# Performance work log

Measured on AMD Instinct MI355X. Metric: run time of the kernel, lower is better.

## Reference

```python
import jax, jax.numpy as jnp
import numpy as np

B = 131072
IN_DIM = 100
H = 256


def setup_inputs() -> dict:
    key = jax.random.key(0)
    ks = jax.random.split(key, 7)
    return {
        "x": jax.random.normal(ks[0], (B, IN_DIM), dtype=jnp.float32),
        "C": jax.random.normal(ks[1], (B, H), dtype=jnp.float32),
        "h": jax.random.normal(ks[2], (B, H), dtype=jnp.float32),
        # stacked gate weights, gate order: i, f, g, o  (equivalent to 8 separate Linears)
        "Wx": jax.random.normal(ks[3], (IN_DIM, 4 * H), dtype=jnp.float32) * 0.05,
        "Wh": jax.random.normal(ks[4], (H, 4 * H), dtype=jnp.float32) * 0.05,
        "bx": jax.random.normal(ks[5], (4 * H,), dtype=jnp.float32) * 0.05,
        "bh": jax.random.normal(ks[6], (4 * H,), dtype=jnp.float32) * 0.05,
    }


def reference(x, C, h, Wx, Wh, bx, bh):
    # two fused GEMMs replace the 8 per-gate Linears (same math)
    gates = (x @ Wx + bx) + (h @ Wh + bh)  # [B, 4H]
    i_pre, f_pre, g_pre, o_pre = jnp.split(gates, 4, axis=-1)
    i = jax.nn.sigmoid(i_pre)
    f = jax.nn.sigmoid(f_pre)
    g = jnp.tanh(g_pre)
    o = jax.nn.sigmoid(o_pre)
    c_out = f * C + i * g
    h_out = o * jnp.tanh(c_out)
    return (c_out, h_out)
```

## Files before the change

### kernel.cpp

```cpp
#include <hip/hip_runtime.h>
#include <stdint.h>


typedef short bf16x8 __attribute__((ext_vector_type(8)));
typedef float f32x4  __attribute__((ext_vector_type(4)));

#define HDIM   256
#define INDIM  100
#define NROWS  131072
#define BT_OFF 0
#define XB_OFF (1048576 / 2)
#define HB_OFF (35651584 / 2)
#define ABUF(b) ((b) * 8192)
#define BBUF(b) (24576 + (b) * 16384)

__device__ __forceinline__ float fexp(float x) {
  return __builtin_amdgcn_exp2f(x * 1.44269504088896340736f);
}
__device__ __forceinline__ float frcp(float x) { return __builtin_amdgcn_rcpf(x); }
__device__ __forceinline__ float sigm(float x) { return frcp(1.0f + fexp(-x)); }
__device__ __forceinline__ float tanh_fast(float x) {
  return 1.0f - 2.0f * frcp(1.0f + fexp(2.0f * x));
}
__device__ __forceinline__ unsigned short f2bf_rne(float f) {
  union { float f; uint32_t u; } v; v.f = f;
  return (unsigned short)((v.u + 0x7FFFu + ((v.u >> 16) & 1u)) >> 16);
}
__device__ __forceinline__ void gl16(const void* g, void* l) {
  __builtin_amdgcn_global_load_lds(
      (const __attribute__((address_space(1))) unsigned int*)g,
      (__attribute__((address_space(3))) unsigned int*)l, 16, 0, 0);
}
#define VMW(N) asm volatile("s_waitcnt vmcnt(" #N ")" ::: "memory")

__global__ void prep_all(const float* __restrict__ X, const float* __restrict__ Hin,
                         const float* __restrict__ Wx, const float* __restrict__ Wh,
                         const float* __restrict__ bxp, const float* __restrict__ bhp,
                         unsigned short* __restrict__ ws) {
  const int b = blockIdx.x, tid = threadIdx.x;
  if (b < 8192) {
    const int t   = b * 256 + tid;
    const int row = t >> 4, k0 = (t & 15) * 8;
    const float* xp = X + (size_t)row * INDIM;
    float4 lo = make_float4(0.f, 0.f, 0.f, 0.f);
    float4 hi = make_float4(0.f, 0.f, 0.f, 0.f);
    if (k0 + 4 <= INDIM) lo = *reinterpret_cast<const float4*>(xp + k0);
    if (k0 + 8 <= INDIM) hi = *reinterpret_cast<const float4*>(xp + k0 + 4);
    float va[8] = {lo.x, lo.y, lo.z, lo.w, hi.x, hi.y, hi.z, hi.w};
    unsigned short o[8];
#pragma unroll
    for (int e = 0; e < 8; ++e) {
      const int k = k0 + e;
      const float f = (k < INDIM) ? va[e] : (k == 127 ? 1.0f : 0.0f);
      o[e] = f2bf_rne(f);
    }
    *reinterpret_cast<bf16x8*>(ws + XB_OFF + (size_t)row * 128 + k0) =
        *reinterpret_cast<bf16x8*>(o);
  } else if (b < 24576) {
    const int t   = (b - 8192) * 256 + tid;
    const int row = t >> 5, k0 = (t & 31) * 8;
    const float* hp = Hin + (size_t)row * HDIM + k0;
    const float4 lo = *reinterpret_cast<const float4*>(hp);
    const float4 hi = *reinterpret_cast<const float4*>(hp + 4);
    unsigned short o[8] = {f2bf_rne(lo.x), f2bf_rne(lo.y), f2bf_rne(lo.z),
                           f2bf_rne(lo.w), f2bf_rne(hi.x), f2bf_rne(hi.y),
                           f2bf_rne(hi.z), f2bf_rne(hi.w)};
    *reinterpret_cast<bf16x8*>(ws + HB_OFF + (size_t)row * 256 + k0) =
        *reinterpret_cast<bf16x8*>(o);
  } else {
    const int unit = (b - 24576) * 4 + (tid >> 6);
    const int lane = tid & 63;
    const int kst  = unit % 12;
    const int fidb = unit / 12;
    const int bn   = fidb >> 3, fid = fidb & 7;
    const int g    = fid >> 1,  wc  = fid & 1;
    const int wcol = g * HDIM + bn * 32 + wc * 16 + (lane & 15);
    const int kb   = kst * 32 + (lane >> 4) * 8;
    unsigned short v[8];
#pragma unroll
    for (int e = 0; e < 8; ++e) {
      const int k = kb + e;
      float f = 0.0f;
      if (k < INDIM)     f = Wx[(size_t)k * 1024 + wcol];
      else if (k == 127) f = bxp[wcol] + bhp[wcol];
      else if (k >= 128) f = Wh[(size_t)(k - 128) * 1024 + wcol];
      v[e] = f2bf_rne(f);
    }
    *reinterpret_cast<bf16x8*>(ws + BT_OFF + (size_t)unit * 512 + lane * 8) =
        *reinterpret_cast<bf16x8*>(v);
  }
}

__global__ __launch_bounds__(512, 2)
void lstm_main(const unsigned short* __restrict__ ws,
               const float* __restrict__ Cin, float* __restrict__ out)
{
  __shared__ unsigned char smem[73728];

  const int tid  = threadIdx.x;
  const int orig = blockIdx.x;
  const int lg   = ((orig & 7) << 9) | (orig >> 3);
  const int mt   = lg >> 2;
  const int bnn  = lg & 3;

  const int lane = tid & 63;
  const int l15  = lane & 15;
  const int kq   = lane >> 4;
  const int wid  = tid >> 6;
  const int wr   = wid >> 2;
  const int wcq  = wid & 3;
  const int ch   = bnn * 64 + wcq * 16 + l15;
  const int sx   = (l15 >> 1) & 3;

  const unsigned short* xb = ws + XB_OFF;
  const unsigned short* hb = ws + HB_OFF;
  const unsigned short* Bt = ws + BT_OFF;

  const int ci = wid * 64 + lane;
  const int r  = ci >> 2;
  const int sc = (ci & 3) ^ ((r >> 1) & 3);
  const unsigned short* xsrc = xb + (size_t)(mt * 128 + r) * 128 + sc * 8;
  const unsigned short* hsrc = hb + (size_t)(mt * 128 + r) * 256 + sc * 8;

  const unsigned short* bsrc[2];
#pragma unroll
  for (int j = 0; j < 2; ++j) {
    const int u  = wid * 2 + j;
    const int gu = (bnn * 2 + (u >> 3)) * 8 + (u & 7);
    bsrc[j] = Bt + (size_t)gu * 12 * 512 + lane * 8;
  }
  const int adst = wid * 1024;
  const int bd0  = (wid * 2 + 0) * 1024;
  const int bd1  = (wid * 2 + 1) * 1024;

  f32x4 acc[4][4];
#pragma unroll
  for (int m = 0; m < 4; ++m)
#pragma unroll
    for (int g = 0; g < 4; ++g)
#pragma unroll
      for (int e = 0; e < 4; ++e) acc[m][g][e] = 0.0f;

  float cvv[4][4];

  auto STAGE = [&](int T) {
    char* Ad = (char*)smem + ABUF(T % 3);
    char* Bd = (char*)smem + BBUF(T % 3);
    if (T < 4) gl16(xsrc + T * 32, Ad + adst);
    else       gl16(hsrc + (T - 4) * 32, Ad + adst);
    gl16(bsrc[0] + T * 512, Bd + bd0);
    gl16(bsrc[1] + T * 512, Bd + bd1);
  };

  auto COMPUTE = [&](int S) {
    const unsigned short* Ab = (const unsigned short*)(smem + ABUF(S % 3));
    const unsigned short* Bb = (const unsigned short*)(smem + BBUF(S % 3));
    bf16x8 afr[4], bfr[4];
#pragma unroll
    for (int m = 0; m < 4; ++m)
      afr[m] = *reinterpret_cast<const bf16x8*>(
          Ab + (wr * 64 + m * 16 + l15) * 32 + ((kq ^ sx) * 8));
#pragma unroll
    for (int g = 0; g < 4; ++g) {
      const int ub = (wcq >> 1) * 8 + g * 2 + (wcq & 1);
      bfr[g] = *reinterpret_cast<const bf16x8*>(Bb + ub * 512 + lane * 8);
    }
#pragma unroll
    for (int m = 0; m < 4; ++m)
#pragma unroll
      for (int g = 0; g < 4; ++g)
        acc[m][g] = __builtin_amdgcn_mfma_f32_16x16x32_bf16(
            afr[m], bfr[g], acc[m][g], 0, 0, 0);
  };

  STAGE(0);
  STAGE(1);

#define STEP(S, KN)                                               \
  do {                                                            \
    VMW(KN);                                                      \
    __builtin_amdgcn_s_barrier();                                 \
    if ((S) + 2 < 12) STAGE((S) + 2);                             \
    if ((S) == 7) {                                               \
      const float* cb =                                           \
          Cin + ((size_t)mt * 128 + wr * 64 + kq * 4) * HDIM + ch;\
      _Pragma("unroll")                                           \
      for (int m = 0; m < 4; ++m)                                 \
        _Pragma("unroll")                                         \
        for (int e = 0; e < 4; ++e)                               \
          cvv[m][e] = __builtin_nontemporal_load(                 \
              cb + (size_t)(m * 16 + e) * HDIM);                  \
    }                                                             \
    COMPUTE(S);                                                   \
  } while (0)

  STEP(0, 3);  STEP(1, 3);  STEP(2, 3);  STEP(3, 3);
  STEP(4, 3);  STEP(5, 3);  STEP(6, 3);  STEP(7, 3);
  STEP(8, 19); STEP(9, 19); STEP(10, 3); STEP(11, 0);
#undef STEP

  float* op  = out + ((size_t)mt * 128 + wr * 64 + kq * 4) * HDIM + ch;
  float* op2 = op + (size_t)NROWS * HDIM;
#pragma unroll
  for (int m = 0; m < 4; ++m) {
#pragma unroll
    for (int e = 0; e < 4; ++e) {
      const float pi = acc[m][0][e];
      const float pf = acc[m][1][e];
      const float pg = acc[m][2][e];
      const float po = acc[m][3][e];
      const float ig = sigm(pi), fg = sigm(pf);
      const float gg = tanh_fast(pg), og = sigm(po);
      const float co = fg * cvv[m][e] + ig * gg;
      const float ho = og * tanh_fast(co);
      __builtin_nontemporal_store(co, op  + (size_t)(m * 16 + e) * HDIM);
      __builtin_nontemporal_store(ho, op2 + (size_t)(m * 16 + e) * HDIM);
    }
  }
}

extern "C" void kernel_launch(void* const* d_in, const int* in_sizes, int n_in,
                              void* d_out, int out_size, void* d_ws, size_t ws_size,
                              hipStream_t stream) {
  const float* x  = (const float*)d_in[0];
  const float* C  = (const float*)d_in[1];
  const float* h  = (const float*)d_in[2];
  const float* Wx = (const float*)d_in[3];
  const float* Wh = (const float*)d_in[4];
  const float* bx = (const float*)d_in[5];
  const float* bh = (const float*)d_in[6];
  float* o = (float*)d_out;
  unsigned short* ws = (unsigned short*)d_ws;

  prep_all<<<dim3(24768), dim3(256), 0, stream>>>(x, h, Wx, Wh, bx, bh, ws);
  lstm_main<<<dim3(4096), dim3(512), 0, stream>>>(ws, C, o);
}
```

Baseline: 193.5 us.

## Switch main GEMM to 32x32x16 MFMA with 4-wave blocks

Replaces the 16x16x32 bf16 MFMA tiles with 32x32x16 tiles, so each wave now computes a 64x32 output per gate. Blocks shrink from 8 to 4 waves, and the weight prepack layout is changed to match the new B-fragment order. Each wave issues more global-to-LDS loads per stage, and the wait counts and C prefetch step are adjusted to fit. The aim is fewer LDS fragment reads per FLOP and better MFMA throughput, at the cost of more accumulator registers per wave and fewer waves per block.

```diff
diff --git a/kernel.cpp b/kernel.cpp
--- a/kernel.cpp
+++ b/kernel.cpp
@@ -3,7 +3,7 @@
 
 
 typedef short bf16x8 __attribute__((ext_vector_type(8)));
-typedef float f32x4  __attribute__((ext_vector_type(4)));
+typedef float f32x16 __attribute__((ext_vector_type(16)));
 
 #define HDIM   256
 #define INDIM  100
@@ -70,12 +70,11 @@
   } else {
     const int unit = (b - 24576) * 4 + (tid >> 6);
     const int lane = tid & 63;
-    const int kst  = unit % 12;
-    const int fidb = unit / 12;
-    const int bn   = fidb >> 3, fid = fidb & 7;
-    const int g    = fid >> 1,  wc  = fid & 1;
-    const int wcol = g * HDIM + bn * 32 + wc * 16 + (lane & 15);
-    const int kb   = kst * 32 + (lane >> 4) * 8;
+    const int kst  = unit % 24;
+    const int g    = (unit / 24) & 3;
+    const int hb32 = unit / 96;
+    const int wcol = g * HDIM + hb32 * 32 + (lane & 31);
+    const int kb   = kst * 16 + (lane >> 5) * 8;
     unsigned short v[8];
 #pragma unroll
     for (int e = 0; e < 8; ++e) {
@@ -91,7 +90,7 @@
   }
 }
 
-__global__ __launch_bounds__(512, 2)
+__global__ __launch_bounds__(256, 2)
 void lstm_main(const unsigned short* __restrict__ ws,
                const float* __restrict__ Cin, float* __restrict__ out)
 {
@@ -104,117 +103,136 @@
   const int bnn  = lg & 3;
 
   const int lane = tid & 63;
-  const int l15  = lane & 15;
-  const int kq   = lane >> 4;
+  const int l31  = lane & 31;
+  const int kh   = lane >> 5;
   const int wid  = tid >> 6;
-  const int wr   = wid >> 2;
-  const int wcq  = wid & 3;
-  const int ch   = bnn * 64 + wcq * 16 + l15;
-  const int sx   = (l15 >> 1) & 3;
+  const int wr   = wid >> 1;
+  const int wc   = wid & 1;
+  const int ch   = bnn * 64 + wc * 32 + l31;
+  const int sx   = (l31 >> 1) & 3;
 
   const unsigned short* xb = ws + XB_OFF;
   const unsigned short* hb = ws + HB_OFF;
   const unsigned short* Bt = ws + BT_OFF;
 
-  const int ci = wid * 64 + lane;
-  const int r  = ci >> 2;
-  const int sc = (ci & 3) ^ ((r >> 1) & 3);
-  const unsigned short* xsrc = xb + (size_t)(mt * 128 + r) * 128 + sc * 8;
-  const unsigned short* hsrc = hb + (size_t)(mt * 128 + r) * 256 + sc * 8;
-
-  const unsigned short* bsrc[2];
+  const unsigned short* xsrc[2];
+  const unsigned short* hsrc[2];
 #pragma unroll
   for (int j = 0; j < 2; ++j) {
-    const int u  = wid * 2 + j;
-    const int gu = (bnn * 2 + (u >> 3)) * 8 + (u & 7);
-    bsrc[j] = Bt + (size_t)gu * 12 * 512 + lane * 8;
-  }
-  const int adst = wid * 1024;
-  const int bd0  = (wid * 2 + 0) * 1024;
-  const int bd1  = (wid * 2 + 1) * 1024;
-
-  f32x4 acc[4][4];
-#pragma unroll
-  for (int m = 0; m < 4; ++m)
+    const int ci = (wid * 2 + j) * 64 + lane;
+    const int r  = ci >> 2;
+    const int sc = (ci & 3) ^ ((r >> 1) & 3);
+    xsrc[j] = xb + (size_t)(mt * 128 + r) * 128 + sc * 8;
+    hsrc[j] = hb + (size_t)(mt * 128 + r) * 256 + sc * 8;
+  }
+  const int ad0 = (wid * 2 + 0) * 1024;
+  const int ad1 = (wid * 2 + 1) * 1024;
+
+  const unsigned short* bsrc[4];
+#pragma unroll
+  for (int j = 0; j < 4; ++j) {
+    const int lu = wid * 4 + j;
+    const int nb = lu >> 3, g = (lu >> 1) & 3, kk = lu & 1;
+    bsrc[j] = Bt + ((size_t)(((bnn * 2 + nb) * 4 + g) * 24) + kk) * 512 +
+              lane * 8;
+  }
+
+  f32x16 acc[2][4];
+#pragma unroll
+  for (int m = 0; m < 2; ++m)
 #pragma unroll
     for (int g = 0; g < 4; ++g)
 #pragma unroll
-      for (int e = 0; e < 4; ++e) acc[m][g][e] = 0.0f;
-
-  float cvv[4][4];
+      for (int e = 0; e < 16; ++e) acc[m][g][e] = 0.0f;
+
+  float cvv[2][16];
 
   auto STAGE = [&](int T) {
     char* Ad = (char*)smem + ABUF(T % 3);
     char* Bd = (char*)smem + BBUF(T % 3);
-    if (T < 4) gl16(xsrc + T * 32, Ad + adst);
-    else       gl16(hsrc + (T - 4) * 32, Ad + adst);
-    gl16(bsrc[0] + T * 512, Bd + bd0);
-    gl16(bsrc[1] + T * 512, Bd + bd1);
+    if (T < 4) {
+      gl16(xsrc[0] + T * 32, Ad + ad0);
+      gl16(xsrc[1] + T * 32, Ad + ad1);
+    } else {
+      gl16(hsrc[0] + (T - 4) * 32, Ad + ad0);
+      gl16(hsrc[1] + (T - 4) * 32, Ad + ad1);
+    }
+#pragma unroll
+    for (int j = 0; j < 4; ++j)
+      gl16(bsrc[j] + T * 1024, Bd + (wid * 4 + j) * 1024);
   };
 
   auto COMPUTE = [&](int S) {
     const unsigned short* Ab = (const unsigned short*)(smem + ABUF(S % 3));
     const unsigned short* Bb = (const unsigned short*)(smem + BBUF(S % 3));
-    bf16x8 afr[4], bfr[4];
-#pragma unroll
-    for (int m = 0; m < 4; ++m)
-      afr[m] = *reinterpret_cast<const bf16x8*>(
-          Ab + (wr * 64 + m * 16 + l15) * 32 + ((kq ^ sx) * 8));
-#pragma unroll
-    for (int g = 0; g < 4; ++g) {
-      const int ub = (wcq >> 1) * 8 + g * 2 + (wcq & 1);
-      bfr[g] = *reinterpret_cast<const bf16x8*>(Bb + ub * 512 + lane * 8);
-    }
-#pragma unroll
-    for (int m = 0; m < 4; ++m)
-#pragma unroll
-      for (int g = 0; g < 4; ++g)
-        acc[m][g] = __builtin_amdgcn_mfma_f32_16x16x32_bf16(
-            afr[m], bfr[g], acc[m][g], 0, 0, 0);
+#pragma unroll
+    for (int kk = 0; kk < 2; ++kk) {
+      bf16x8 afr[2], bfr[4];
+#pragma unroll
+      for (int m = 0; m < 2; ++m) {
+        const int row   = wr * 64 + m * 32 + l31;
+        const int chunk = (kk * 2 + kh) ^ sx;
+        afr[m] = *reinterpret_cast<const bf16x8*>(Ab + row * 32 + chunk * 8);
+      }
+#pragma unroll
+      for (int g = 0; g < 4; ++g) {
+        const int u = wc * 8 + g * 2 + kk;
+        bfr[g] = *reinterpret_cast<const bf16x8*>(Bb + u * 512 + lane * 8);
+      }
+#pragma unroll
+      for (int m = 0; m < 2; ++m)
+#pragma unroll
+        for (int g = 0; g < 4; ++g)
+          acc[m][g] = __builtin_amdgcn_mfma_f32_32x32x16_bf16(
+              afr[m], bfr[g], acc[m][g], 0, 0, 0);
+    }
   };
 
   STAGE(0);
   STAGE(1);
 
-#define STEP(S, KN)                                               \
-  do {                                                            \
-    VMW(KN);                                                      \
-    __builtin_amdgcn_s_barrier();                                 \
-    if ((S) + 2 < 12) STAGE((S) + 2);                             \
-    if ((S) == 7) {                                               \
-      const float* cb =                                           \
-          Cin + ((size_t)mt * 128 + wr * 64 + kq * 4) * HDIM + ch;\
-      _Pragma("unroll")                                           \
-      for (int m = 0; m < 4; ++m)                                 \
-        _Pragma("unroll")                                         \
-        for (int e = 0; e < 4; ++e)                               \
-          cvv[m][e] = __builtin_nontemporal_load(                 \
-              cb + (size_t)(m * 16 + e) * HDIM);                  \
-    }                                                             \
-    COMPUTE(S);                                                   \
+#define STEP(S, KN)                                                \
+  do {                                                             \
+    VMW(KN);                                                       \
+    __builtin_amdgcn_s_barrier();                                  \
+    if ((S) + 2 < 12) STAGE((S) + 2);                              \
+    if ((S) == 8) {                                                \
+      const float* cb =                                            \
+          Cin + ((size_t)mt * 128 + wr * 64 + 4 * kh) * HDIM + ch; \
+      _Pragma("unroll")                                            \
+      for (int m = 0; m < 2; ++m)                                  \
+        _Pragma("unroll")                                          \
+        for (int rg = 0; rg < 16; ++rg) {                          \
+          const int roff = m * 32 + (rg & 3) + 8 * (rg >> 2);      \
+          cvv[m][rg] = __builtin_nontemporal_load(                 \
+              cb + (size_t)roff * HDIM);                           \
+        }                                                          \
+    }                                                              \
+    COMPUTE(S);                                                    \
   } while (0)
 
-  STEP(0, 3);  STEP(1, 3);  STEP(2, 3);  STEP(3, 3);
-  STEP(4, 3);  STEP(5, 3);  STEP(6, 3);  STEP(7, 3);
-  STEP(8, 19); STEP(9, 19); STEP(10, 3); STEP(11, 0);
+  STEP(0, 6);  STEP(1, 6);  STEP(2, 6);  STEP(3, 6);
+  STEP(4, 6);  STEP(5, 6);  STEP(6, 6);  STEP(7, 6);
+  STEP(8, 6);  STEP(9, 38); STEP(10, 38); STEP(11, 0);
 #undef STEP
 
-  float* op  = out + ((size_t)mt * 128 + wr * 64 + kq * 4) * HDIM + ch;
+  float* op  = out + ((size_t)mt * 128 + wr * 64 + 4 * kh) * HDIM + ch;
   float* op2 = op + (size_t)NROWS * HDIM;
 #pragma unroll
-  for (int m = 0; m < 4; ++m) {
-#pragma unroll
-    for (int e = 0; e < 4; ++e) {
-      const float pi = acc[m][0][e];
-      const float pf = acc[m][1][e];
-      const float pg = acc[m][2][e];
-      const float po = acc[m][3][e];
+  for (int m = 0; m < 2; ++m) {
+#pragma unroll
+    for (int rg = 0; rg < 16; ++rg) {
+      const int roff = m * 32 + (rg & 3) + 8 * (rg >> 2);
+      const float pi = acc[m][0][rg];
+      const float pf = acc[m][1][rg];
+      const float pg = acc[m][2][rg];
+      const float po = acc[m][3][rg];
       const float ig = sigm(pi), fg = sigm(pf);
       const float gg = tanh_fast(pg), og = sigm(po);
-      const float co = fg * cvv[m][e] + ig * gg;
+      const float co = fg * cvv[m][rg] + ig * gg;
       const float ho = og * tanh_fast(co);
-      __builtin_nontemporal_store(co, op  + (size_t)(m * 16 + e) * HDIM);
-      __builtin_nontemporal_store(ho, op2 + (size_t)(m * 16 + e) * HDIM);
+      __builtin_nontemporal_store(co, op  + (size_t)roff * HDIM);
+      __builtin_nontemporal_store(ho, op2 + (size_t)roff * HDIM);
     }
   }
 }
@@ -233,5 +251,5 @@
   unsigned short* ws = (unsigned short*)d_ws;
 
   prep_all<<<dim3(24768), dim3(256), 0, stream>>>(x, h, Wx, Wh, bx, bh, ws);
-  lstm_main<<<dim3(4096), dim3(512), 0, stream>>>(ws, C, o);
-}
+  lstm_main<<<dim3(4096), dim3(256), 0, stream>>>(ws, C, o);
+}
```

After: 188.9 us, median of 2. 1.02x faster.
